# Kernel tuning notes

Measured on AMD Instinct MI355X. Metric: run time of the kernel, lower is better.

## Reference

```python
import jax, jax.numpy as jnp
import numpy as np
import math

D = 1024
H = 16
DH = D // H
FF = 4096
B, S = 2, 2048


def _layernorm(x, g, b, eps=1e-5):
    mu = jnp.mean(x, axis=-1, keepdims=True)
    var = jnp.var(x, axis=-1, keepdims=True)
    return (x - mu) * jax.lax.rsqrt(var + eps) * g + b


def _gelu_tanh(x):
    # 0.5*x*(1+tanh(sqrt(2/pi)*(x+0.044715*x^3)))
    c = math.sqrt(2.0 / math.pi)
    return 0.5 * x * (1.0 + jnp.tanh(c * (x + 0.044715 * x ** 3)))


def setup_inputs() -> dict:
    key = jax.random.key(0)
    ks = jax.random.split(key, 8)
    s = 0.02
    return {
        "x": jax.random.normal(ks[0], (B, S, D), dtype=jnp.float32),
        "ln1_g": jnp.ones((D,), jnp.float32),
        "ln1_b": jnp.zeros((D,), jnp.float32),
        "Wqkv": jax.random.normal(ks[1], (D, 3 * D), jnp.float32) * s,
        "bqkv": jnp.zeros((3 * D,), jnp.float32),
        "Wo": jax.random.normal(ks[2], (D, D), jnp.float32) * s,
        "bo": jnp.zeros((D,), jnp.float32),
        "ln2_g": jnp.ones((D,), jnp.float32),
        "ln2_b": jnp.zeros((D,), jnp.float32),
        "W1": jax.random.normal(ks[3], (D, FF), jnp.float32) * s,
        "b1": jnp.zeros((FF,), jnp.float32),
        "W2": jax.random.normal(ks[4], (FF, D), jnp.float32) * s,
        "b2": jnp.zeros((D,), jnp.float32),
    }


def reference(x, ln1_g, ln1_b, Wqkv, bqkv, Wo, bo, ln2_g, ln2_b, W1, b1, W2, b2):
    b, s, d = x.shape
    h = _layernorm(x, ln1_g, ln1_b)
    qkv = h @ Wqkv + bqkv                       # [B,S,3D]
    q, k, v = jnp.split(qkv, 3, axis=-1)
    q = q.reshape(b, s, H, DH).transpose(0, 2, 1, 3)   # [B,H,S,Dh]
    k = k.reshape(b, s, H, DH).transpose(0, 2, 1, 3)
    v = v.reshape(b, s, H, DH).transpose(0, 2, 1, 3)
    scores = jnp.einsum("bhqd,bhkd->bhqk", q, k) / math.sqrt(DH)
    probs = jax.nn.softmax(scores, axis=-1)
    attn = jnp.einsum("bhqk,bhkd->bhqd", probs, v)     # [B,H,S,Dh]
    attn = attn.transpose(0, 2, 1, 3).reshape(b, s, d)
    attn = attn @ Wo + bo
    x = x + attn
    m = _layernorm(x, ln2_g, ln2_b)
    m = _gelu_tanh(m @ W1 + b1) @ W2 + b2
    return x + m
```

## Files before the change

kernel.cpp:

```cpp
#include <hip/hip_runtime.h>
#include <hip/hip_bf16.h>
#include <cstdint>

#define D_ 1024
#define H_ 16
#define DH_ 64
#define FF_ 4096
#define B_ 2
#define S_ 2048
#define MR_ (B_ * S_)

typedef __bf16 bf16x8 __attribute__((ext_vector_type(8)));
typedef __bf16 bf16x4 __attribute__((ext_vector_type(4)));
typedef float f32x4 __attribute__((ext_vector_type(4)));
typedef float f32x16 __attribute__((ext_vector_type(16)));

__device__ __forceinline__ void g2lds16(const void* g, void* l) {
  __builtin_amdgcn_global_load_lds(
      (__attribute__((address_space(1))) void*)(uintptr_t)g,
      (__attribute__((address_space(3))) void*)(uint32_t)(uintptr_t)l,
      16, 0, 0);
}

__device__ __forceinline__ unsigned pkbf16(float lo, float hi) {
  unsigned r;
  asm("v_cvt_pk_bf16_f32 %0, %1, %2" : "=v"(r) : "v"(lo), "v"(hi));
  return r;
}

__device__ __forceinline__ float fexp2(float x) {
  return __builtin_amdgcn_exp2f(x);
}

__global__ __launch_bounds__(256) void transpose_cvt(
    const float* __restrict__ W, __hip_bfloat16* __restrict__ Wt, int K, int N) {
  __shared__ float t[32][33];
  int bx = blockIdx.x * 32;
  int by = blockIdx.y * 32;
  int tx = threadIdx.x, ty = threadIdx.y;
#pragma unroll
  for (int i = 0; i < 4; ++i)
    t[ty + 8 * i][tx] = W[(size_t)(by + ty + 8 * i) * N + bx + tx];
  __syncthreads();
#pragma unroll
  for (int i = 0; i < 4; ++i)
    Wt[(size_t)(bx + ty + 8 * i) * K + by + tx] = __float2bfloat16(t[tx][ty + 8 * i]);
}

__global__ __launch_bounds__(256) void ln_kernel(
    const float* __restrict__ x, const float* __restrict__ g,
    const float* __restrict__ b, __hip_bfloat16* __restrict__ out) {
  int row = blockIdx.x;
  const float4* xr = (const float4*)(x + (size_t)row * D_);
  float4 v = xr[threadIdx.x];
  float s = v.x + v.y + v.z + v.w;
  float ss = v.x * v.x + v.y * v.y + v.z * v.z + v.w * v.w;
#pragma unroll
  for (int m = 1; m < 64; m <<= 1) {
    s += __shfl_xor(s, m);
    ss += __shfl_xor(ss, m);
  }
  __shared__ float rs[4], rss[4];
  int wave = threadIdx.x >> 6, lane = threadIdx.x & 63;
  if (lane == 0) { rs[wave] = s; rss[wave] = ss; }
  __syncthreads();
  s = rs[0] + rs[1] + rs[2] + rs[3];
  ss = rss[0] + rss[1] + rss[2] + rss[3];
  float mean = s * (1.0f / D_);
  float var = ss * (1.0f / D_) - mean * mean;
  float inv = rsqrtf(var + 1e-5f);
  int c = threadIdx.x * 4;
  float4 gv = ((const float4*)g)[threadIdx.x];
  float4 bv = ((const float4*)b)[threadIdx.x];
  __hip_bfloat16* o = out + (size_t)row * D_ + c;
  o[0] = __float2bfloat16((v.x - mean) * inv * gv.x + bv.x);
  o[1] = __float2bfloat16((v.y - mean) * inv * gv.y + bv.y);
  o[2] = __float2bfloat16((v.z - mean) * inv * gv.z + bv.z);
  o[3] = __float2bfloat16((v.w - mean) * inv * gv.w + bv.w);
}

template <int EPI>
__global__ __launch_bounds__(256) void gemm4(
    const __hip_bfloat16* __restrict__ A, const __hip_bfloat16* __restrict__ Bt,
    const float* __restrict__ bias, const float* __restrict__ resid,
    void* __restrict__ outp, __hip_bfloat16* __restrict__ vt, int M, int N, int K) {
  constexpr int BM = 128, BN = 128, MF = 4, NF = 4;
  __shared__ alignas(16) __hip_bfloat16 sA[2][BM * 64];
  __shared__ alignas(16) __hip_bfloat16 sB[2][BN * 64];
  const int tid = threadIdx.x;
  const int lane = tid & 63, wave = tid >> 6;
  const int l15 = lane & 15, l4 = lane >> 4;
  const int wr = wave >> 1, wc = wave & 1;
  const int csw = (l15 & 7) << 3;

  const int gx = gridDim.x;
  int nwg = gx * gridDim.y;
  int flat = blockIdx.y * gx + blockIdx.x;
  int cpx = nwg >> 3;
  int swz = (flat & 7) * cpx + (flat >> 3);
  const int m0 = (swz / gx) * BM, n0 = (swz % gx) * BN;

  f32x4 z = {0.f, 0.f, 0.f, 0.f};
  f32x4 acc[MF][NF];
#pragma unroll
  for (int i = 0; i < MF; ++i)
#pragma unroll
    for (int j = 0; j < NF; ++j) acc[i][j] = z;

  auto stage = [&](int bu, int kt) {
#pragma unroll
    for (int it = 0; it < 4; ++it) {
      int idx = it * 256 + tid;
      int r = idx >> 3, c = (idx & 7) * 8;
      int cs = c ^ ((r & 7) << 3);
      g2lds16(A + (size_t)(m0 + r) * K + kt + cs, (void*)(&sA[bu][idx * 8]));
      g2lds16(Bt + (size_t)(n0 + r) * K + kt + cs, (void*)(&sB[bu][idx * 8]));
    }
  };

  const int nk = K / 64;
  stage(0, 0);
  asm volatile("s_waitcnt vmcnt(0)" ::: "memory");
  __builtin_amdgcn_s_barrier();

  for (int j = 0; j < nk; ++j) {
    const int cur = j & 1;
    if (j + 1 < nk) stage(cur ^ 1, (j + 1) * 64);

    __builtin_amdgcn_s_setprio(1);
#pragma unroll
    for (int kk = 0; kk < 2; ++kk) {
      int col = (kk * 32 + l4 * 8) ^ csw;
      bf16x8 bfr[NF];
#pragma unroll
      for (int nf = 0; nf < NF; ++nf)
        bfr[nf] = *(const bf16x8*)(&sB[cur][(wc * 64 + nf * 16 + l15) * 64 + col]);
#pragma unroll
      for (int mf = 0; mf < MF; ++mf) {
        bf16x8 af = *(const bf16x8*)(&sA[cur][(wr * 64 + mf * 16 + l15) * 64 + col]);
#pragma unroll
        for (int nf = 0; nf < NF; ++nf)
          acc[mf][nf] =
              __builtin_amdgcn_mfma_f32_16x16x32_bf16(af, bfr[nf], acc[mf][nf], 0, 0, 0);
      }
    }
    __builtin_amdgcn_s_setprio(0);

    asm volatile("s_waitcnt lgkmcnt(0)" ::: "memory");
    __builtin_amdgcn_sched_barrier(0);
    asm volatile("s_waitcnt vmcnt(0)" ::: "memory");
    __builtin_amdgcn_s_barrier();
    asm volatile("" ::: "memory");
  }

#pragma unroll
  for (int mf = 0; mf < MF; ++mf) {
#pragma unroll
    for (int nf = 0; nf < NF; ++nf) {
      int col = n0 + wc * 64 + nf * 16 + l15;
      float bv = bias[col];
      if (EPI == 3 && col >= 2 * D_) {
        int d = col - 2 * D_;
        int srow0 = m0 + wr * 64 + mf * 16 + l4 * 4;
        int bb = srow0 >> 11, s0 = srow0 & (S_ - 1);
        bf16x4 ov;
#pragma unroll
        for (int j = 0; j < 4; ++j) ov[j] = (__bf16)(acc[mf][nf][j] + bv);
        *(bf16x4*)(vt + ((size_t)(bb * H_ + (d >> 6)) * DH_ + (d & 63)) * S_ + s0) = ov;
      } else {
#pragma unroll
        for (int j = 0; j < 4; ++j) {
          int row = m0 + wr * 64 + mf * 16 + l4 * 4 + j;
          size_t o = (size_t)row * N + col;
          float v = acc[mf][nf][j] + bv;
          if (EPI == 0 || EPI == 3) {
            ((__hip_bfloat16*)outp)[o] = __float2bfloat16(v);
          } else if (EPI == 1) {
            ((float*)outp)[o] = v + resid[o];
          } else {
            float a = 0.7978845608028654f * (v + 0.044715f * v * v * v);
            a = fminf(fmaxf(a, -15.f), 15.f);
            float e = __expf(2.f * a);
            float th = (e - 1.f) / (e + 1.f);
            ((__hip_bfloat16*)outp)[o] = __float2bfloat16(0.5f * v * (1.f + th));
          }
        }
      }
    }
  }
}

template <int EPI>
__global__ __launch_bounds__(512, 1) void gemm256(
    const __hip_bfloat16* __restrict__ A, const __hip_bfloat16* __restrict__ Bt,
    const float* __restrict__ bias, const float* __restrict__ resid,
    void* __restrict__ outp, int M, int N, int K) {
  constexpr int BM = 256, BN = 256, MF = 8, NF = 4, WN = 4;
  __shared__ alignas(16) __hip_bfloat16 sA[2][BM * 64];
  __shared__ alignas(16) __hip_bfloat16 sB[2][BN * 64];
  const int tid = threadIdx.x;
  const int lane = tid & 63, wave = tid >> 6;
  const int l15 = lane & 15, l4 = lane >> 4;
  const int wr = wave / WN, wc = wave % WN;
  const int csw = (l15 & 7) << 3;

  const int gx = gridDim.x;
  int nwg = gx * gridDim.y;
  int flat = blockIdx.y * gx + blockIdx.x;
  int cpx = nwg >> 3;
  int swz = (flat & 7) * cpx + (flat >> 3);
  const int m0 = (swz / gx) * BM, n0 = (swz % gx) * BN;

  f32x4 z = {0.f, 0.f, 0.f, 0.f};
  f32x4 acc[MF][NF];
#pragma unroll
  for (int i = 0; i < MF; ++i)
#pragma unroll
    for (int j = 0; j < NF; ++j) acc[i][j] = z;

  auto stage = [&](int bu, int kt) {
#pragma unroll
    for (int it = 0; it < 4; ++it) {
      int idx = it * 512 + tid;
      int r = idx >> 3, c = (idx & 7) * 8;
      int cs = c ^ ((r & 7) << 3);
      g2lds16(A + (size_t)(m0 + r) * K + kt + cs, (void*)(&sA[bu][idx * 8]));
      g2lds16(Bt + (size_t)(n0 + r) * K + kt + cs, (void*)(&sB[bu][idx * 8]));
    }
  };

  const int nk = K / 64;
  stage(0, 0);
  asm volatile("s_waitcnt vmcnt(0)" ::: "memory");
  __builtin_amdgcn_s_barrier();

  for (int j = 0; j < nk; ++j) {
    const int cur = j & 1;
    if (j + 1 < nk) stage(cur ^ 1, (j + 1) * 64);

    __builtin_amdgcn_s_setprio(1);
#pragma unroll
    for (int kk = 0; kk < 2; ++kk) {
      int col = (kk * 32 + l4 * 8) ^ csw;
      bf16x8 bfr[NF];
#pragma unroll
      for (int nf = 0; nf < NF; ++nf)
        bfr[nf] = *(const bf16x8*)(&sB[cur][(wc * 64 + nf * 16 + l15) * 64 + col]);
#pragma unroll
      for (int mf = 0; mf < MF; ++mf) {
        bf16x8 af = *(const bf16x8*)(&sA[cur][(wr * 128 + mf * 16 + l15) * 64 + col]);
#pragma unroll
        for (int nf = 0; nf < NF; ++nf)
          acc[mf][nf] =
              __builtin_amdgcn_mfma_f32_16x16x32_bf16(af, bfr[nf], acc[mf][nf], 0, 0, 0);
      }
    }
    __builtin_amdgcn_s_setprio(0);

    asm volatile("s_waitcnt lgkmcnt(0)" ::: "memory");
    __builtin_amdgcn_sched_barrier(0);
    asm volatile("s_waitcnt vmcnt(0)" ::: "memory");
    __builtin_amdgcn_s_barrier();
    asm volatile("" ::: "memory");
  }

#pragma unroll
  for (int mf = 0; mf < MF; ++mf) {
#pragma unroll
    for (int nf = 0; nf < NF; ++nf) {
      int col = n0 + wc * 64 + nf * 16 + l15;
      float bv = bias[col];
#pragma unroll
      for (int j = 0; j < 4; ++j) {
        int row = m0 + wr * 128 + mf * 16 + l4 * 4 + j;
        size_t o = (size_t)row * N + col;
        float v = acc[mf][nf][j] + bv;
        if (EPI == 0) {
          ((__hip_bfloat16*)outp)[o] = __float2bfloat16(v);
        } else if (EPI == 1) {
          ((float*)outp)[o] = v + resid[o];
        } else {
          float a = 0.7978845608028654f * (v + 0.044715f * v * v * v);
          a = fminf(fmaxf(a, -15.f), 15.f);
          float e = __expf(2.f * a);
          float th = (e - 1.f) / (e + 1.f);
          ((__hip_bfloat16*)outp)[o] = __float2bfloat16(0.5f * v * (1.f + th));
        }
      }
    }
  }
}

template <int EPI>
__global__ __launch_bounds__(512) void gemmr3(
    const __hip_bfloat16* __restrict__ A, const __hip_bfloat16* __restrict__ Bt,
    const float* __restrict__ bias, const float* __restrict__ resid,
    void* __restrict__ outp, int M, int N, int K) {
  constexpr int BM = 128, BN = 128, MF = 4, NF = 2, WN = 4;
  __shared__ alignas(16) __hip_bfloat16 sA[3][BM * 64];
  __shared__ alignas(16) __hip_bfloat16 sB[3][BN * 64];
  const int tid = threadIdx.x;
  const int lane = tid & 63, wave = tid >> 6;
  const int l15 = lane & 15, l4 = lane >> 4;
  const int wr = wave / WN, wc = wave % WN;
  const int csw = (l15 & 7) << 3;

  const int gx = gridDim.x;
  int nwg = gx * gridDim.y;
  int flat = blockIdx.y * gx + blockIdx.x;
  int cpx = nwg >> 3;
  int swz = (flat & 7) * cpx + (flat >> 3);
  const int m0 = (swz / gx) * BM, n0 = (swz % gx) * BN;

  f32x4 z = {0.f, 0.f, 0.f, 0.f};
  f32x4 acc[MF][NF];
#pragma unroll
  for (int i = 0; i < MF; ++i)
#pragma unroll
    for (int j = 0; j < NF; ++j) acc[i][j] = z;

  auto stage = [&](int bu, int kt) {
#pragma unroll
    for (int it = 0; it < 2; ++it) {
      int idx = it * 512 + tid;
      int r = idx >> 3, c = (idx & 7) * 8;
      int cs = c ^ ((r & 7) << 3);
      g2lds16(A + (size_t)(m0 + r) * K + kt + cs, (void*)(&sA[bu][idx * 8]));
      g2lds16(Bt + (size_t)(n0 + r) * K + kt + cs, (void*)(&sB[bu][idx * 8]));
    }
  };

  const int nk = K / 64;
  stage(0, 0);
  stage(1, 64);
  asm volatile("s_waitcnt vmcnt(4)" ::: "memory");
  __builtin_amdgcn_s_barrier();

  int bu = 0, bu2 = 2;
  for (int j = 0; j < nk; ++j) {
    const bool pf = (j + 2) < nk;
    if (pf) stage(bu2, (j + 2) * 64);

    __builtin_amdgcn_s_setprio(1);
#pragma unroll
    for (int kk = 0; kk < 2; ++kk) {
      int col = (kk * 32 + l4 * 8) ^ csw;
      bf16x8 bfr[NF];
#pragma unroll
      for (int nf = 0; nf < NF; ++nf)
        bfr[nf] = *(const bf16x8*)(&sB[bu][(wc * NF * 16 + nf * 16 + l15) * 64 + col]);
#pragma unroll
      for (int mf = 0; mf < MF; ++mf) {
        bf16x8 af = *(const bf16x8*)(&sA[bu][(wr * MF * 16 + mf * 16 + l15) * 64 + col]);
#pragma unroll
        for (int nf = 0; nf < NF; ++nf)
          acc[mf][nf] =
              __builtin_amdgcn_mfma_f32_16x16x32_bf16(af, bfr[nf], acc[mf][nf], 0, 0, 0);
      }
    }
    __builtin_amdgcn_s_setprio(0);

    asm volatile("s_waitcnt lgkmcnt(0)" ::: "memory");
    __builtin_amdgcn_sched_barrier(0);
    if (pf)
      asm volatile("s_waitcnt vmcnt(4)" ::: "memory");
    else
      asm volatile("s_waitcnt vmcnt(0)" ::: "memory");
    __builtin_amdgcn_s_barrier();
    asm volatile("" ::: "memory");
    bu = (bu == 2) ? 0 : bu + 1;
    bu2 = (bu2 == 2) ? 0 : bu2 + 1;
  }

#pragma unroll
  for (int mf = 0; mf < MF; ++mf) {
#pragma unroll
    for (int nf = 0; nf < NF; ++nf) {
      int col = n0 + wc * NF * 16 + nf * 16 + l15;
      float bv = bias[col];
#pragma unroll
      for (int j = 0; j < 4; ++j) {
        int row = m0 + wr * MF * 16 + mf * 16 + l4 * 4 + j;
        size_t o = (size_t)row * N + col;
        float v = acc[mf][nf][j] + bv;
        if (EPI == 0) {
          ((__hip_bfloat16*)outp)[o] = __float2bfloat16(v);
        } else if (EPI == 1) {
          ((float*)outp)[o] = v + resid[o];
        } else {
          float a = 0.7978845608028654f * (v + 0.044715f * v * v * v);
          a = fminf(fmaxf(a, -15.f), 15.f);
          float e = __expf(2.f * a);
          float th = (e - 1.f) / (e + 1.f);
          ((__hip_bfloat16*)outp)[o] = __float2bfloat16(0.5f * v * (1.f + th));
        }
      }
    }
  }
}

__global__ __launch_bounds__(256, 2) void attn_kernel(
    const __hip_bfloat16* __restrict__ qkv, const __hip_bfloat16* __restrict__ vT,
    __hip_bfloat16* __restrict__ out) {
  __shared__ alignas(16) __hip_bfloat16 sK[2][64 * 64];
  __shared__ alignas(16) __hip_bfloat16 sV[2][64 * 64];
  const int tid = threadIdx.x, lane = tid & 63, wave = tid >> 6;
  const int l31 = lane & 31, hi = lane >> 5;
  const int bh = blockIdx.y, b = bh >> 4, h = bh & 15;
  const int q0 = blockIdx.x * 256;
  const int rsw = (l31 & 7) << 3;
  const float k2 = 0.125f * 1.44269504f;

  bf16x8 qfA[4], qfB[4];
  {
    int qrA = q0 + wave * 64 + l31;
    const size_t qbA = ((size_t)(b * S_ + qrA)) * (3 * D_) + h * DH_;
    const size_t qbB = qbA + (size_t)32 * (3 * D_);
#pragma unroll
    for (int ks = 0; ks < 4; ++ks) {
      bf16x8 qa = *(const bf16x8*)(qkv + qbA + ks * 16 + hi * 8);
      bf16x8 qb = *(const bf16x8*)(qkv + qbB + ks * 16 + hi * 8);
#pragma unroll
      for (int i = 0; i < 8; ++i) {
        qa[i] = (__bf16)((float)qa[i] * k2);
        qb[i] = (__bf16)((float)qb[i] * k2);
      }
      qfA[ks] = qa;
      qfB[ks] = qb;
    }
  }

  bf16x8 onesb;
#pragma unroll
  for (int i = 0; i < 8; ++i) onesb[i] = (__bf16)1.0f;

  f32x16 Z16;
#pragma unroll
  for (int r = 0; r < 16; ++r) Z16[r] = 0.f;

  f32x16 accA0 = Z16, accA1 = Z16, accLA = Z16;
  f32x16 accB0 = Z16, accB1 = Z16, accLB = Z16;

  const __hip_bfloat16* kg = qkv + (size_t)b * S_ * (3 * D_) + D_ + h * DH_;
  const __hip_bfloat16* vg = vT + (size_t)bh * DH_ * S_;

  auto stage = [&](int bu, int kv0) {
#pragma unroll
    for (int it = 0; it < 2; ++it) {
      int idx = it * 256 + tid;
      int r = idx >> 3;
      int c = (idx & 7) * 8;
      int cs = c ^ ((r & 7) << 3);
      g2lds16(kg + (size_t)(kv0 + r) * (3 * D_) + cs, (void*)(&sK[bu][idx * 8]));
      g2lds16(vg + (size_t)r * S_ + kv0 + cs, (void*)(&sV[bu][idx * 8]));
    }
  };

  stage(0, 0);
  const int NT = S_ / 64;

  for (int t = 0; t < NT; ++t) {
    const int cur = t & 1;
    __syncthreads();
    if (t + 1 < NT) stage(cur ^ 1, (t + 1) * 64);

    f32x16 sfA0, sfA1, sfB0, sfB1;
    __builtin_amdgcn_s_setprio(1);
    {
      int colsw = (hi * 8) ^ rsw;
      bf16x8 kf0 = *(const bf16x8*)(&sK[cur][l31 * 64 + colsw]);
      bf16x8 kf1 = *(const bf16x8*)(&sK[cur][(32 + l31) * 64 + colsw]);
      sfA0 = __builtin_amdgcn_mfma_f32_32x32x16_bf16(kf0, qfA[0], Z16, 0, 0, 0);
      sfA1 = __builtin_amdgcn_mfma_f32_32x32x16_bf16(kf1, qfA[0], Z16, 0, 0, 0);
      sfB0 = __builtin_amdgcn_mfma_f32_32x32x16_bf16(kf0, qfB[0], Z16, 0, 0, 0);
      sfB1 = __builtin_amdgcn_mfma_f32_32x32x16_bf16(kf1, qfB[0], Z16, 0, 0, 0);
    }
#pragma unroll
    for (int ks = 1; ks < 4; ++ks) {
      int colsw = (ks * 16 + hi * 8) ^ rsw;
      bf16x8 kf0 = *(const bf16x8*)(&sK[cur][l31 * 64 + colsw]);
      bf16x8 kf1 = *(const bf16x8*)(&sK[cur][(32 + l31) * 64 + colsw]);
      sfA0 = __builtin_amdgcn_mfma_f32_32x32x16_bf16(kf0, qfA[ks], sfA0, 0, 0, 0);
      sfA1 = __builtin_amdgcn_mfma_f32_32x32x16_bf16(kf1, qfA[ks], sfA1, 0, 0, 0);
      sfB0 = __builtin_amdgcn_mfma_f32_32x32x16_bf16(kf0, qfB[ks], sfB0, 0, 0, 0);
      sfB1 = __builtin_amdgcn_mfma_f32_32x32x16_bf16(kf1, qfB[ks], sfB1, 0, 0, 0);
    }
    __builtin_amdgcn_s_setprio(0);

    bf16x8 paA[4], paB[4];
#pragma unroll
    for (int g = 0; g < 2; ++g) {
      const f32x16& s0 = g ? sfB0 : sfA0;
      const f32x16& s1 = g ? sfB1 : sfA1;
      bf16x8* pa = g ? paB : paA;
#pragma unroll
      for (int kb = 0; kb < 2; ++kb) {
        const f32x16& s16 = kb ? s1 : s0;
#pragma unroll
        for (int ksb = 0; ksb < 2; ++ksb) {
          float p0 = fexp2(s16[8 * ksb + 0]);
          float p1 = fexp2(s16[8 * ksb + 1]);
          float p2 = fexp2(s16[8 * ksb + 2]);
          float p3 = fexp2(s16[8 * ksb + 3]);
          float p4 = fexp2(s16[8 * ksb + 4]);
          float p5 = fexp2(s16[8 * ksb + 5]);
          float p6 = fexp2(s16[8 * ksb + 6]);
          float p7 = fexp2(s16[8 * ksb + 7]);
          unsigned wa = pkbf16(p0, p1), wb = pkbf16(p2, p3);
          unsigned wc = pkbf16(p4, p5), wd = pkbf16(p6, p7);
          auto r1 = __builtin_amdgcn_permlane32_swap(wa, wc, false, false);
          auto r2 = __builtin_amdgcn_permlane32_swap(wb, wd, false, false);
          union { unsigned u[4]; bf16x8 v; } w;
          w.u[0] = r1[0]; w.u[1] = r2[0]; w.u[2] = r1[1]; w.u[3] = r2[1];
          pa[kb * 2 + ksb] = w.v;
        }
      }
    }

    __builtin_amdgcn_s_setprio(1);
#pragma unroll
    for (int ksg = 0; ksg < 4; ++ksg) {
      int colsw = (ksg * 16 + hi * 8) ^ rsw;
      bf16x8 vf0 = *(const bf16x8*)(&sV[cur][l31 * 64 + colsw]);
      bf16x8 vf1 = *(const bf16x8*)(&sV[cur][(32 + l31) * 64 + colsw]);
      accA0 = __builtin_amdgcn_mfma_f32_32x32x16_bf16(paA[ksg], vf0, accA0, 0, 0, 0);
      accA1 = __builtin_amdgcn_mfma_f32_32x32x16_bf16(paA[ksg], vf1, accA1, 0, 0, 0);
      accLA = __builtin_amdgcn_mfma_f32_32x32x16_bf16(paA[ksg], onesb, accLA, 0, 0, 0);
      accB0 = __builtin_amdgcn_mfma_f32_32x32x16_bf16(paB[ksg], vf0, accB0, 0, 0, 0);
      accB1 = __builtin_amdgcn_mfma_f32_32x32x16_bf16(paB[ksg], vf1, accB1, 0, 0, 0);
      accLB = __builtin_amdgcn_mfma_f32_32x32x16_bf16(paB[ksg], onesb, accLB, 0, 0, 0);
    }
    __builtin_amdgcn_s_setprio(0);
  }

#pragma unroll
  for (int r = 0; r < 16; ++r) {
    int qrow = (r & 3) + 8 * (r >> 2) + 4 * hi;
    size_t obA = ((size_t)(b * S_ + q0 + wave * 64 + qrow)) * D_ + h * DH_ + l31;
    size_t obB = obA + (size_t)32 * D_;
    float irA = 1.0f / accLA[r];
    float irB = 1.0f / accLB[r];
    out[obA] = __float2bfloat16(accA0[r] * irA);
    out[obA + 32] = __float2bfloat16(accA1[r] * irA);
    out[obB] = __float2bfloat16(accB0[r] * irB);
    out[obB + 32] = __float2bfloat16(accB1[r] * irB);
  }
}

extern "C" void kernel_launch(void* const* d_in, const int* in_sizes, int n_in,
                              void* d_out, int out_size, void* d_ws, size_t ws_size,
                              hipStream_t stream) {
  const float* x = (const float*)d_in[0];
  const float* ln1_g = (const float*)d_in[1];
  const float* ln1_b = (const float*)d_in[2];
  const float* Wqkv = (const float*)d_in[3];
  const float* bqkv = (const float*)d_in[4];
  const float* Wo = (const float*)d_in[5];
  const float* bo = (const float*)d_in[6];
  const float* ln2_g = (const float*)d_in[7];
  const float* ln2_b = (const float*)d_in[8];
  const float* W1 = (const float*)d_in[9];
  const float* b1 = (const float*)d_in[10];
  const float* W2 = (const float*)d_in[11];
  const float* b2 = (const float*)d_in[12];
  float* out = (float*)d_out;

  char* ws = (char*)d_ws;
  size_t off = 0;
  auto alloc = [&](size_t bytes) {
    void* p = ws + off;
    off += (bytes + 255) & ~(size_t)255;
    return p;
  };
  __hip_bfloat16* WqkvT = (__hip_bfloat16*)alloc((size_t)3 * D_ * D_ * 2);
  __hip_bfloat16* WoT = (__hip_bfloat16*)alloc((size_t)D_ * D_ * 2);
  __hip_bfloat16* W1T = (__hip_bfloat16*)alloc((size_t)FF_ * D_ * 2);
  __hip_bfloat16* W2T = (__hip_bfloat16*)alloc((size_t)D_ * FF_ * 2);
  __hip_bfloat16* h = (__hip_bfloat16*)alloc((size_t)MR_ * D_ * 2);
  __hip_bfloat16* qkv = (__hip_bfloat16*)alloc((size_t)MR_ * FF_ * 2);
  __hip_bfloat16* ff = qkv;
  __hip_bfloat16* vT = (__hip_bfloat16*)alloc((size_t)B_ * H_ * DH_ * S_ * 2);
  __hip_bfloat16* attn_out = (__hip_bfloat16*)alloc((size_t)MR_ * D_ * 2);

  dim3 tb(32, 8);
  transpose_cvt<<<dim3(3 * D_ / 32, D_ / 32), tb, 0, stream>>>(Wqkv, WqkvT, D_, 3 * D_);
  transpose_cvt<<<dim3(D_ / 32, D_ / 32), tb, 0, stream>>>(Wo, WoT, D_, D_);
  transpose_cvt<<<dim3(FF_ / 32, D_ / 32), tb, 0, stream>>>(W1, W1T, D_, FF_);
  transpose_cvt<<<dim3(D_ / 32, FF_ / 32), tb, 0, stream>>>(W2, W2T, FF_, D_);
  ln_kernel<<<MR_, 256, 0, stream>>>(x, ln1_g, ln1_b, h);
  gemm4<3><<<dim3(3 * D_ / 128, MR_ / 128), 256, 0, stream>>>(
      h, WqkvT, bqkv, nullptr, qkv, vT, MR_, 3 * D_, D_);
  attn_kernel<<<dim3(S_ / 256, B_ * H_), 256, 0, stream>>>(qkv, vT, attn_out);
  gemmr3<1><<<dim3(D_ / 128, MR_ / 128), 512, 0, stream>>>(
      attn_out, WoT, bo, x, out, MR_, D_, D_);
  ln_kernel<<<MR_, 256, 0, stream>>>(out, ln2_g, ln2_b, h);
  gemm256<2><<<dim3(FF_ / 256, MR_ / 256), 512, 0, stream>>>(
      h, W1T, b1, nullptr, ff, MR_, FF_, D_);
  gemmr3<1><<<dim3(D_ / 128, MR_ / 128), 512, 0, stream>>>(
      ff, W2T, b2, out, out, MR_, D_, FF_);
}
```

Baseline: 209.4 us.

## Merge weight transposes into one launch and use 128x64 tiles for output GEMMs

The four weight transpose/convert launches become one 1D-grid kernel that picks the matrix from the block index, which removes three launches. The Wo and W2 GEMMs move from a 128x128, 512-thread, triple-buffered kernel to a 128x64, 256-thread, double-buffered kernel, launching twice as many workgroups (512 instead of 256) to fill the CUs better for N=1024. The trade-off is less prefetch depth and lower reuse per tile, especially for the K=4096 W2 GEMM.

After: 204.6 us. 1.02x faster.

```diff
diff --git a/kernel.cpp b/kernel.cpp
--- a/kernel.cpp
+++ b/kernel.cpp
@@ -32,12 +32,24 @@
   return __builtin_amdgcn_exp2f(x);
 }
 
-__global__ __launch_bounds__(256) void transpose_cvt(
-    const float* __restrict__ W, __hip_bfloat16* __restrict__ Wt, int K, int N) {
+__global__ __launch_bounds__(256) void transpose_all(
+    const float* __restrict__ W0, __hip_bfloat16* __restrict__ T0,
+    const float* __restrict__ W1p, __hip_bfloat16* __restrict__ T1,
+    const float* __restrict__ W2p, __hip_bfloat16* __restrict__ T2,
+    const float* __restrict__ W3p, __hip_bfloat16* __restrict__ T3) {
   __shared__ float t[32][33];
-  int bx = blockIdx.x * 32;
-  int by = blockIdx.y * 32;
-  int tx = threadIdx.x, ty = threadIdx.y;
+  int ti = blockIdx.x;
+  const float* W;
+  __hip_bfloat16* Wt;
+  int K, N, loc;
+  if (ti < 3072)      { W = W0;  Wt = T0; K = 1024; N = 3072; loc = ti; }
+  else if (ti < 4096) { W = W1p; Wt = T1; K = 1024; N = 1024; loc = ti - 3072; }
+  else if (ti < 8192) { W = W2p; Wt = T2; K = 1024; N = 4096; loc = ti - 4096; }
+  else                { W = W3p; Wt = T3; K = 4096; N = 1024; loc = ti - 8192; }
+  int ntn = N >> 5;
+  int bx = (loc % ntn) * 32;
+  int by = (loc / ntn) * 32;
+  int tx = threadIdx.x & 31, ty = threadIdx.x >> 5;
 #pragma unroll
   for (int i = 0; i < 4; ++i)
     t[ty + 8 * i][tx] = W[(size_t)(by + ty + 8 * i) * N + bx + tx];
@@ -191,17 +203,17 @@
 }
 
 template <int EPI>
-__global__ __launch_bounds__(512, 1) void gemm256(
+__global__ __launch_bounds__(256) void gemm64(
     const __hip_bfloat16* __restrict__ A, const __hip_bfloat16* __restrict__ Bt,
     const float* __restrict__ bias, const float* __restrict__ resid,
     void* __restrict__ outp, int M, int N, int K) {
-  constexpr int BM = 256, BN = 256, MF = 8, NF = 4, WN = 4;
+  constexpr int BM = 128, BN = 64, MF = 4, NF = 2;
   __shared__ alignas(16) __hip_bfloat16 sA[2][BM * 64];
   __shared__ alignas(16) __hip_bfloat16 sB[2][BN * 64];
   const int tid = threadIdx.x;
   const int lane = tid & 63, wave = tid >> 6;
   const int l15 = lane & 15, l4 = lane >> 4;
-  const int wr = wave / WN, wc = wave % WN;
+  const int wr = wave >> 1, wc = wave & 1;
   const int csw = (l15 & 7) << 3;
 
   const int gx = gridDim.x;
@@ -221,10 +233,16 @@
   auto stage = [&](int bu, int kt) {
 #pragma unroll
     for (int it = 0; it < 4; ++it) {
-      int idx = it * 512 + tid;
+      int idx = it * 256 + tid;
       int r = idx >> 3, c = (idx & 7) * 8;
       int cs = c ^ ((r & 7) << 3);
       g2lds16(A + (size_t)(m0 + r) * K + kt + cs, (void*)(&sA[bu][idx * 8]));
+    }
+#pragma unroll
+    for (int it = 0; it < 2; ++it) {
+      int idx = it * 256 + tid;
+      int r = idx >> 3, c = (idx & 7) * 8;
+      int cs = c ^ ((r & 7) << 3);
       g2lds16(Bt + (size_t)(n0 + r) * K + kt + cs, (void*)(&sB[bu][idx * 8]));
     }
   };
@@ -245,10 +263,10 @@
       bf16x8 bfr[NF];
 #pragma unroll
       for (int nf = 0; nf < NF; ++nf)
-        bfr[nf] = *(const bf16x8*)(&sB[cur][(wc * 64 + nf * 16 + l15) * 64 + col]);
+        bfr[nf] = *(const bf16x8*)(&sB[cur][(wc * 32 + nf * 16 + l15) * 64 + col]);
 #pragma unroll
       for (int mf = 0; mf < MF; ++mf) {
-        bf16x8 af = *(const bf16x8*)(&sA[cur][(wr * 128 + mf * 16 + l15) * 64 + col]);
+        bf16x8 af = *(const bf16x8*)(&sA[cur][(wr * 64 + mf * 16 + l15) * 64 + col]);
 #pragma unroll
         for (int nf = 0; nf < NF; ++nf)
           acc[mf][nf] =
@@ -268,11 +286,11 @@
   for (int mf = 0; mf < MF; ++mf) {
 #pragma unroll
     for (int nf = 0; nf < NF; ++nf) {
-      int col = n0 + wc * 64 + nf * 16 + l15;
+      int col = n0 + wc * 32 + nf * 16 + l15;
       float bv = bias[col];
 #pragma unroll
       for (int j = 0; j < 4; ++j) {
-        int row = m0 + wr * 128 + mf * 16 + l4 * 4 + j;
+        int row = m0 + wr * 64 + mf * 16 + l4 * 4 + j;
         size_t o = (size_t)row * N + col;
         float v = acc[mf][nf][j] + bv;
         if (EPI == 0) {
@@ -292,13 +310,13 @@
 }
 
 template <int EPI>
-__global__ __launch_bounds__(512) void gemmr3(
+__global__ __launch_bounds__(512, 1) void gemm256(
     const __hip_bfloat16* __restrict__ A, const __hip_bfloat16* __restrict__ Bt,
     const float* __restrict__ bias, const float* __restrict__ resid,
     void* __restrict__ outp, int M, int N, int K) {
-  constexpr int BM = 128, BN = 128, MF = 4, NF = 2, WN = 4;
-  __shared__ alignas(16) __hip_bfloat16 sA[3][BM * 64];
-  __shared__ alignas(16) __hip_bfloat16 sB[3][BN * 64];
+  constexpr int BM = 256, BN = 256, MF = 8, NF = 4, WN = 4;
+  __shared__ alignas(16) __hip_bfloat16 sA[2][BM * 64];
+  __shared__ alignas(16) __hip_bfloat16 sB[2][BN * 64];
   const int tid = threadIdx.x;
   const int lane = tid & 63, wave = tid >> 6;
   const int l15 = lane & 15, l4 = lane >> 4;
@@ -321,7 +339,7 @@
 
   auto stage = [&](int bu, int kt) {
 #pragma unroll
-    for (int it = 0; it < 2; ++it) {
+    for (int it = 0; it < 4; ++it) {
       int idx = it * 512 + tid;
       int r = idx >> 3, c = (idx & 7) * 8;
       int cs = c ^ ((r & 7) << 3);
@@ -332,14 +350,12 @@
 
   const int nk = K / 64;
   stage(0, 0);
-  stage(1, 64);
-  asm volatile("s_waitcnt vmcnt(4)" ::: "memory");
+  asm volatile("s_waitcnt vmcnt(0)" ::: "memory");
   __builtin_amdgcn_s_barrier();
 
-  int bu = 0, bu2 = 2;
   for (int j = 0; j < nk; ++j) {
-    const bool pf = (j + 2) < nk;
-    if (pf) stage(bu2, (j + 2) * 64);
+    const int cur = j & 1;
+    if (j + 1 < nk) stage(cur ^ 1, (j + 1) * 64);
 
     __builtin_amdgcn_s_setprio(1);
 #pragma unroll
@@ -348,10 +364,10 @@
       bf16x8 bfr[NF];
 #pragma unroll
       for (int nf = 0; nf < NF; ++nf)
-        bfr[nf] = *(const bf16x8*)(&sB[bu][(wc * NF * 16 + nf * 16 + l15) * 64 + col]);
+        bfr[nf] = *(const bf16x8*)(&sB[cur][(wc * 64 + nf * 16 + l15) * 64 + col]);
 #pragma unroll
       for (int mf = 0; mf < MF; ++mf) {
-        bf16x8 af = *(const bf16x8*)(&sA[bu][(wr * MF * 16 + mf * 16 + l15) * 64 + col]);
+        bf16x8 af = *(const bf16x8*)(&sA[cur][(wr * 128 + mf * 16 + l15) * 64 + col]);
 #pragma unroll
         for (int nf = 0; nf < NF; ++nf)
           acc[mf][nf] =
@@ -362,25 +378,20 @@
 
     asm volatile("s_waitcnt lgkmcnt(0)" ::: "memory");
     __builtin_amdgcn_sched_barrier(0);
-    if (pf)
-      asm volatile("s_waitcnt vmcnt(4)" ::: "memory");
-    else
-      asm volatile("s_waitcnt vmcnt(0)" ::: "memory");
+    asm volatile("s_waitcnt vmcnt(0)" ::: "memory");
     __builtin_amdgcn_s_barrier();
     asm volatile("" ::: "memory");
-    bu = (bu == 2) ? 0 : bu + 1;
-    bu2 = (bu2 == 2) ? 0 : bu2 + 1;
   }
 
 #pragma unroll
   for (int mf = 0; mf < MF; ++mf) {
 #pragma unroll
     for (int nf = 0; nf < NF; ++nf) {
-      int col = n0 + wc * NF * 16 + nf * 16 + l15;
+      int col = n0 + wc * 64 + nf * 16 + l15;
       float bv = bias[col];
 #pragma unroll
       for (int j = 0; j < 4; ++j) {
-        int row = m0 + wr * MF * 16 + mf * 16 + l4 * 4 + j;
+        int row = m0 + wr * 128 + mf * 16 + l4 * 4 + j;
         size_t o = (size_t)row * N + col;
         float v = acc[mf][nf][j] + bv;
         if (EPI == 0) {
@@ -582,20 +593,16 @@
   __hip_bfloat16* vT = (__hip_bfloat16*)alloc((size_t)B_ * H_ * DH_ * S_ * 2);
   __hip_bfloat16* attn_out = (__hip_bfloat16*)alloc((size_t)MR_ * D_ * 2);
 
-  dim3 tb(32, 8);
-  transpose_cvt<<<dim3(3 * D_ / 32, D_ / 32), tb, 0, stream>>>(Wqkv, WqkvT, D_, 3 * D_);
-  transpose_cvt<<<dim3(D_ / 32, D_ / 32), tb, 0, stream>>>(Wo, WoT, D_, D_);
-  transpose_cvt<<<dim3(FF_ / 32, D_ / 32), tb, 0, stream>>>(W1, W1T, D_, FF_);
-  transpose_cvt<<<dim3(D_ / 32, FF_ / 32), tb, 0, stream>>>(W2, W2T, FF_, D_);
+  transpose_all<<<dim3(12288), 256, 0, stream>>>(Wqkv, WqkvT, Wo, WoT, W1, W1T, W2, W2T);
   ln_kernel<<<MR_, 256, 0, stream>>>(x, ln1_g, ln1_b, h);
   gemm4<3><<<dim3(3 * D_ / 128, MR_ / 128), 256, 0, stream>>>(
       h, WqkvT, bqkv, nullptr, qkv, vT, MR_, 3 * D_, D_);
   attn_kernel<<<dim3(S_ / 256, B_ * H_), 256, 0, stream>>>(qkv, vT, attn_out);
-  gemmr3<1><<<dim3(D_ / 128, MR_ / 128), 512, 0, stream>>>(
+  gemm64<1><<<dim3(D_ / 64, MR_ / 128), 256, 0, stream>>>(
       attn_out, WoT, bo, x, out, MR_, D_, D_);
   ln_kernel<<<MR_, 256, 0, stream>>>(out, ln2_g, ln2_b, h);
   gemm256<2><<<dim3(FF_ / 256, MR_ / 256), 512, 0, stream>>>(
       h, W1T, b1, nullptr, ff, MR_, FF_, D_);
-  gemmr3<1><<<dim3(D_ / 128, MR_ / 128), 512, 0, stream>>>(
+  gemm64<1><<<dim3(D_ / 64, MR_ / 128), 256, 0, stream>>>(
       ff, W2T, b2, out, out, MR_, D_, FF_);
 }
```
